# Kernel optimization log

Hardware: AMD Instinct MI355X
Metric: run time of the kernel (lower is better)

Reference implementation:

```python
import jax, jax.numpy as jnp
import numpy as np

EMB_DIM = 1024
N_HEAD = 16
HEAD_DIM = EMB_DIM // N_HEAD


def setup_inputs() -> dict:
    key = jax.random.key(0)
    k1, k2, k3, k4, k5 = jax.random.split(key, 5)
    x = jax.random.normal(k1, (4, 2048, EMB_DIM), dtype=jnp.float32)
    s = 1.0 / np.sqrt(EMB_DIM)
    W_qkv = jax.random.uniform(k2, (3 * EMB_DIM, EMB_DIM), minval=-s, maxval=s, dtype=jnp.float32)
    b_qkv = jax.random.uniform(k3, (3 * EMB_DIM,), minval=-s, maxval=s, dtype=jnp.float32)
    W_proj = jax.random.uniform(k4, (EMB_DIM, EMB_DIM), minval=-s, maxval=s, dtype=jnp.float32)
    b_proj = jax.random.uniform(k5, (EMB_DIM,), minval=-s, maxval=s, dtype=jnp.float32)
    return {"x": x, "W_qkv": W_qkv, "b_qkv": b_qkv, "W_proj": W_proj, "b_proj": b_proj}


def reference(x, W_qkv, b_qkv, W_proj, b_proj):
    B, S, E = x.shape
    H, D = N_HEAD, HEAD_DIM
    qkv = x @ W_qkv.T + b_qkv  # [B,S,3E]
    q, k, v = jnp.split(qkv, 3, axis=-1)
    # [B,S,E] -> [B,H,S,D]
    q = q.reshape(B, S, H, D).transpose(0, 2, 1, 3)
    k = k.reshape(B, S, H, D).transpose(0, 2, 1, 3)
    v = v.reshape(B, S, H, D).transpose(0, 2, 1, 3)
    scale = 1.0 / jnp.sqrt(jnp.asarray(D, dtype=x.dtype))
    scores = jnp.einsum('bhqd,bhkd->bhqk', q, k) * scale
    causal = jnp.tril(jnp.ones((S, S), dtype=bool))
    scores = jnp.where(causal, scores, jnp.asarray(-jnp.inf, dtype=scores.dtype))
    attn = jax.nn.softmax(scores, axis=-1)
    y = jnp.einsum('bhqk,bhkd->bhqd', attn, v)  # [B,H,S,D]
    y = y.transpose(0, 2, 1, 3).reshape(B, S, E)
    return y @ W_proj.T + b_proj
```

## Files before the change

kernel.cpp:

```cpp
#include <hip/hip_runtime.h>
#include <hip/hip_bf16.h>

typedef __attribute__((ext_vector_type(4))) float f32x4;
typedef __attribute__((ext_vector_type(16))) float f32x16;
typedef __attribute__((ext_vector_type(8))) __bf16 bf16x8;
typedef __attribute__((ext_vector_type(4))) unsigned int u32x4;

#define EMB 1024
#define NHEAD 16
#define HDIM 64
#define SEQ 2048
#define BATCH 4
#define NTOK 8192

__device__ __forceinline__ unsigned short f2bf(float f) {
    unsigned int u = __builtin_bit_cast(unsigned int, f);
    u = (u + 0x7fffu + ((u >> 16) & 1u)) >> 16;
    return (unsigned short)u;
}

__device__ __forceinline__ unsigned int cvt2_bf16(float lo, float hi) {
    unsigned short a = __builtin_bit_cast(unsigned short, (__bf16)lo);
    unsigned short b = __builtin_bit_cast(unsigned short, (__bf16)hi);
    return (unsigned int)a | ((unsigned int)b << 16);
}

__device__ __forceinline__ void permlane32_swap(unsigned int &x, unsigned int &y) {
    asm volatile("v_permlane32_swap_b32 %0, %1" : "+v"(x), "+v"(y));
}

__device__ __forceinline__ void async_copy16(const ushort* g, ushort* l) {
    __builtin_amdgcn_global_load_lds(
        (const __attribute__((address_space(1))) void*)g,
        (__attribute__((address_space(3))) void*)l,
        16, 0, 0);
}

__global__ void cvt_f32_bf16(const float4* __restrict__ in, ushort* __restrict__ out, int n4) {
    int i = blockIdx.x * 256 + threadIdx.x;
    if (i < n4) {
        float4 v = in[i];
        ushort4 o;
        o.x = f2bf(v.x); o.y = f2bf(v.y); o.z = f2bf(v.z); o.w = f2bf(v.w);
        ((ushort4*)out)[i] = o;
    }
}

#define GEMM_STAGE64(Asrc, Bsrc, m0, n0, kt)                                      \
    {                                                                             \
        _Pragma("unroll")                                                         \
        for (int j = 0; j < 2; ++j) {                                             \
            int row = wave * 32 + j * 16 + (lane >> 2);                           \
            int kc  = (lane & 3) ^ ((row >> 1) & 3);                              \
            const ushort* asrc = Asrc + (size_t)(m0 + row) * EMB + kt + kc * 8;   \
            const ushort* bsrc = Bsrc + (size_t)(n0 + row) * EMB + kt + kc * 8;   \
            async_copy16(asrc,      As0 + (wave * 32 + j * 16) * 32);             \
            async_copy16(asrc + 32, As1 + (wave * 32 + j * 16) * 32);             \
            async_copy16(bsrc,      Bs0 + (wave * 32 + j * 16) * 32);             \
            async_copy16(bsrc + 32, Bs1 + (wave * 32 + j * 16) * 32);             \
        }                                                                         \
    }

#define GEMM_BODY64(Asrc, Bsrc, m0, n0)                                           \
    f32x4 acc[4][4] = {};                                                         \
    for (int kt = 0; kt < EMB; kt += 64) {                                        \
        GEMM_STAGE64(Asrc, Bsrc, m0, n0, kt)                                      \
        __syncthreads();                                                          \
        _Pragma("unroll")                                                         \
        for (int hf = 0; hf < 2; ++hf) {                                          \
            const ushort* Ah = hf ? As1 : As0;                                    \
            const ushort* Bh = hf ? Bs1 : Bs0;                                    \
            bf16x8 a[4], b[4];                                                    \
            _Pragma("unroll")                                                     \
            for (int i = 0; i < 4; ++i) {                                         \
                int r = wm + i * 16 + col;                                        \
                a[i] = *(const bf16x8*)&Ah[r * 32 + (quad ^ ((r >> 1) & 3)) * 8]; \
                int c = wn + i * 16 + col;                                        \
                b[i] = *(const bf16x8*)&Bh[c * 32 + (quad ^ ((c >> 1) & 3)) * 8]; \
            }                                                                     \
            _Pragma("unroll")                                                     \
            for (int i = 0; i < 4; ++i)                                           \
                _Pragma("unroll")                                                 \
                for (int j = 0; j < 4; ++j)                                       \
                    acc[i][j] = __builtin_amdgcn_mfma_f32_16x16x32_bf16(          \
                        a[i], b[j], acc[i][j], 0, 0, 0);                          \
        }                                                                         \
        __syncthreads();                                                          \
    }

__global__ __launch_bounds__(256) void gemm_qk(
    const ushort* __restrict__ A,
    const ushort* __restrict__ W,
    const float*  __restrict__ bias,
    ushort* __restrict__ Qb, ushort* __restrict__ Kb)
{
    __shared__ ushort As0[128 * 32];
    __shared__ ushort As1[128 * 32];
    __shared__ ushort Bs0[128 * 32];
    __shared__ ushort Bs1[128 * 32];
    const int tid  = threadIdx.x;
    const int lane = tid & 63;
    const int wave = tid >> 6;
    const int col  = lane & 15;
    const int quad = lane >> 4;
    const int m0 = blockIdx.x * 128;
    const int n0 = blockIdx.y * 128;
    const int wm = (wave >> 1) * 64;
    const int wn = (wave & 1) * 64;

    GEMM_BODY64(A, W, m0, n0)

    #pragma unroll
    for (int i = 0; i < 4; ++i)
        #pragma unroll
        for (int j = 0; j < 4; ++j)
            #pragma unroll
            for (int r = 0; r < 4; ++r) {
                int m = m0 + wm + i * 16 + quad * 4 + r;
                int n = n0 + wn + j * 16 + col;
                float v = acc[i][j][r] + bias[n];
                unsigned short bv = f2bf(v);
                int e = n & 1023;
                int h = e >> 6, d = e & 63;
                int b = m >> 11, s = m & 2047;
                size_t bh = (size_t)(b * NHEAD + h);
                if (n < 1024) Qb[(bh * SEQ + s) * HDIM + d] = bv;
                else          Kb[(bh * SEQ + s) * HDIM + d] = bv;
            }
}

__global__ __launch_bounds__(256) void gemm_vt(
    const ushort* __restrict__ Wv,
    const ushort* __restrict__ X,
    const float*  __restrict__ bias,
    ushort* __restrict__ Vtx)
{
    __shared__ ushort As0[128 * 32];
    __shared__ ushort As1[128 * 32];
    __shared__ ushort Bs0[128 * 32];
    __shared__ ushort Bs1[128 * 32];
    const int tid  = threadIdx.x;
    const int lane = tid & 63;
    const int wave = tid >> 6;
    const int col  = lane & 15;
    const int quad = lane >> 4;
    const int m0 = blockIdx.x * 128;
    const int n0 = blockIdx.y * 128;
    const int wm = (wave >> 1) * 64;
    const int wn = (wave & 1) * 64;

    GEMM_BODY64(Wv, X, m0, n0)

    #pragma unroll
    for (int i = 0; i < 4; ++i)
        #pragma unroll
        for (int j = 0; j < 4; ++j)
            #pragma unroll
            for (int r = 0; r < 4; ++r) {
                int m = m0 + wm + i * 16 + quad * 4 + r;
                int n = n0 + wn + j * 16 + col;
                Vtx[(size_t)m * NTOK + n] = f2bf(acc[i][j][r] + bias[m]);
            }
}

__global__ __launch_bounds__(256) void gemm_proj(
    const ushort* __restrict__ A,
    const ushort* __restrict__ W,
    const float*  __restrict__ bias,
    float* __restrict__ out)
{
    __shared__ ushort As0[128 * 32];
    __shared__ ushort As1[128 * 32];
    __shared__ ushort Bs0[128 * 32];
    __shared__ ushort Bs1[128 * 32];
    const int tid  = threadIdx.x;
    const int lane = tid & 63;
    const int wave = tid >> 6;
    const int col  = lane & 15;
    const int quad = lane >> 4;
    const int m0 = blockIdx.x * 128;
    const int n0 = blockIdx.y * 128;
    const int wm = (wave >> 1) * 64;
    const int wn = (wave & 1) * 64;

    GEMM_BODY64(A, W, m0, n0)

    #pragma unroll
    for (int i = 0; i < 4; ++i)
        #pragma unroll
        for (int j = 0; j < 4; ++j)
            #pragma unroll
            for (int r = 0; r < 4; ++r) {
                int m = m0 + wm + i * 16 + quad * 4 + r;
                int n = n0 + wn + j * 16 + col;
                out[(size_t)m * EMB + n] = acc[i][j][r] + bias[n];
            }
}

__device__ __forceinline__ void attn_qtile(
    int qt, int b, int h, int lane, int wave,
    const ushort* __restrict__ Qh, const ushort* __restrict__ Kh,
    const ushort* __restrict__ Vh, ushort* __restrict__ Yb,
    ushort* __restrict__ Ks0, ushort* __restrict__ Ks1, ushort* __restrict__ Vs)
{
    const int ql = lane & 31;
    const int hi = lane >> 5;
    const int q0 = qt * 128 + wave * 32;
    const int qrow = q0 + ql;
    const float SC = 0.125f * 1.44269504f;

    bf16x8 qb[4];
    #pragma unroll
    for (int c = 0; c < 4; ++c)
        qb[c] = *(const bf16x8*)(Qh + (size_t)qrow * HDIM + c * 16 + hi * 8);

    f32x16 o2[2] = {};
    float lrun = 0.f;

    const int nk = qt + 1;
    for (int kt = 0; kt < nk; ++kt) {
        const int k0 = kt * 128;
        const bool last = (kt == nk - 1);

        {
            int srow = wave * 16 + (lane >> 2);
            #pragma unroll
            for (int rr = 0; rr < 2; ++rr) {
                int r = rr * 64 + srow;
                int kc = (lane & 3) ^ ((r >> 1) & 3);
                const ushort* src = Kh + (size_t)(k0 + r) * HDIM + kc * 8;
                async_copy16(src,      Ks0 + (rr * 64 + wave * 16) * 32);
                async_copy16(src + 32, Ks1 + (rr * 64 + wave * 16) * 32);
            }
            int kc = (lane & 3) ^ ((srow >> 1) & 3);
            const ushort* vsrc = Vh + (size_t)srow * NTOK + k0 + kc * 8;
            #pragma unroll
            for (int kq = 0; kq < 4; ++kq)
                async_copy16(vsrc + kq * 32, Vs + kq * 2048 + (wave * 16) * 32);
        }
        __syncthreads();

        f32x16 st[4];
        #pragma unroll
        for (int t = 0; t < 4; ++t) {
            f32x16 acc = {};
            #pragma unroll
            for (int c = 0; c < 4; ++c) {
                int row = t * 32 + ql;
                int swz = ((c & 1) * 2 + hi) ^ ((row >> 1) & 3);
                const ushort* Kbase = (c < 2) ? Ks0 : Ks1;
                bf16x8 kf = *(const bf16x8*)&Kbase[row * 32 + swz * 8];
                acc = __builtin_amdgcn_mfma_f32_32x32x16_bf16(kf, qb[c], acc, 0, 0, 0);
            }
            st[t] = acc;
        }

        if (last) {
            #pragma unroll
            for (int t = 0; t < 4; ++t)
                #pragma unroll
                for (int r = 0; r < 16; ++r) {
                    float pv = __builtin_amdgcn_exp2f(st[t][r] * SC);
                    int key = k0 + t * 32 + (r & 3) + 8 * (r >> 2) + 4 * hi;
                    pv = (key <= qrow) ? pv : 0.f;
                    st[t][r] = pv;
                    lrun += pv;
                }
        } else {
            #pragma unroll
            for (int t = 0; t < 4; ++t)
                #pragma unroll
                for (int r = 0; r < 16; ++r) {
                    float pv = __builtin_amdgcn_exp2f(st[t][r] * SC);
                    st[t][r] = pv;
                    lrun += pv;
                }
        }

        #pragma unroll
        for (int t = 0; t < 4; ++t) {
            unsigned int Ap[4], Bp[4];
            #pragma unroll
            for (int m = 0; m < 4; ++m) {
                Ap[m] = cvt2_bf16(st[t][4 * m],     st[t][4 * m + 1]);
                Bp[m] = cvt2_bf16(st[t][4 * m + 2], st[t][4 * m + 3]);
            }
            #pragma unroll
            for (int kc = 0; kc < 2; ++kc) {
                unsigned int xa = Ap[2 * kc], ya = Ap[2 * kc + 1];
                unsigned int xb = Bp[2 * kc], yb = Bp[2 * kc + 1];
                permlane32_swap(xa, ya);
                permlane32_swap(xb, yb);
                u32x4 pw; pw[0] = xa; pw[1] = xb; pw[2] = ya; pw[3] = yb;
                bf16x8 pf = __builtin_bit_cast(bf16x8, pw);
                #pragma unroll
                for (int dt = 0; dt < 2; ++dt) {
                    int row = dt * 32 + ql;
                    int swz = (kc * 2 + hi) ^ ((row >> 1) & 3);
                    bf16x8 vf = *(const bf16x8*)&Vs[t * 2048 + row * 32 + swz * 8];
                    o2[dt] = __builtin_amdgcn_mfma_f32_32x32x16_bf16(vf, pf, o2[dt], 0, 0, 0);
                }
            }
        }
        __syncthreads();
    }

    lrun += __shfl_xor(lrun, 32, 64);
    float inv = 1.f / lrun;
    size_t rbase = ((size_t)(b * SEQ + qrow)) * EMB + h * HDIM;
    #pragma unroll
    for (int dt = 0; dt < 2; ++dt)
        #pragma unroll
        for (int m = 0; m < 4; ++m) {
            int d = dt * 32 + 8 * m + 4 * hi;
            ushort4 s4;
            s4.x = f2bf(o2[dt][4 * m]     * inv);
            s4.y = f2bf(o2[dt][4 * m + 1] * inv);
            s4.z = f2bf(o2[dt][4 * m + 2] * inv);
            s4.w = f2bf(o2[dt][4 * m + 3] * inv);
            *(ushort4*)(Yb + rbase + d) = s4;
        }
}

__global__ __launch_bounds__(256, 2) void attn(
    const ushort* __restrict__ Qb, const ushort* __restrict__ Kb,
    const ushort* __restrict__ Vtx, ushort* __restrict__ Yb)
{
    __shared__ ushort Ks0[128 * 32];
    __shared__ ushort Ks1[128 * 32];
    __shared__ ushort Vs[4 * 64 * 32];
    const int lane = threadIdx.x & 63;
    const int wave = threadIdx.x >> 6;
    const int bh   = blockIdx.x & 63;
    const int pr   = blockIdx.x >> 6;

    const int b = bh >> 4, h = bh & 15;
    const ushort* Qh = Qb + (size_t)bh * SEQ * HDIM;
    const ushort* Kh = Kb + (size_t)bh * SEQ * HDIM;
    const ushort* Vh = Vtx + (size_t)(h * HDIM) * NTOK + b * SEQ;

    attn_qtile(15 - pr, b, h, lane, wave, Qh, Kh, Vh, Yb, Ks0, Ks1, Vs);
    __syncthreads();
    attn_qtile(pr,      b, h, lane, wave, Qh, Kh, Vh, Yb, Ks0, Ks1, Vs);
}

extern "C" void kernel_launch(void* const* d_in, const int* in_sizes, int n_in,
                              void* d_out, int out_size, void* d_ws, size_t ws_size,
                              hipStream_t stream) {
    const float* x      = (const float*)d_in[0];
    const float* W_qkv  = (const float*)d_in[1];
    const float* b_qkv  = (const float*)d_in[2];
    const float* W_proj = (const float*)d_in[3];
    const float* b_proj = (const float*)d_in[4];
    float* out = (float*)d_out;

    ushort* ws     = (ushort*)d_ws;
    ushort* Xb     = ws;
    ushort* Yb     = ws;
    ushort* Wqkvb  = ws + 8388608;
    ushort* Wprojb = ws + 11534336;
    ushort* Qb     = ws + 12582912;
    ushort* Kb     = ws + 20971520;
    ushort* Vtx    = ws + 29360128;

    cvt_f32_bf16<<<8192, 256, 0, stream>>>((const float4*)x,      Xb,     2097152);
    cvt_f32_bf16<<<3072, 256, 0, stream>>>((const float4*)W_qkv,  Wqkvb,  786432);
    cvt_f32_bf16<<<1024, 256, 0, stream>>>((const float4*)W_proj, Wprojb, 262144);

    gemm_qk<<<dim3(64, 16), 256, 0, stream>>>(Xb, Wqkvb, b_qkv, Qb, Kb);
    gemm_vt<<<dim3(8, 64), 256, 0, stream>>>(Wqkvb + (size_t)2048 * EMB, Xb,
                                             b_qkv + 2048, Vtx);
    attn<<<512, 256, 0, stream>>>(Qb, Kb, Vtx, Yb);
    gemm_proj<<<dim3(64, 8), 256, 0, stream>>>(Yb, Wprojb, b_proj, out);
}
```

Baseline: 244.7 us.

## Enlarge QK GEMM tiles to 256x256 with 512 threads and fuse conversion kernels

```diff
diff --git a/kernel.cpp b/kernel.cpp
--- a/kernel.cpp
+++ b/kernel.cpp
@@ -36,14 +36,23 @@
         16, 0, 0);
 }
 
-__global__ void cvt_f32_bf16(const float4* __restrict__ in, ushort* __restrict__ out, int n4) {
+#define XN4 2097152
+#define WQN4 786432
+#define WPN4 262144
+__global__ void cvt_all(const float4* __restrict__ x, const float4* __restrict__ wqkv,
+                        const float4* __restrict__ wproj,
+                        ushort* __restrict__ xb, ushort* __restrict__ wqkvb,
+                        ushort* __restrict__ wprojb) {
     int i = blockIdx.x * 256 + threadIdx.x;
-    if (i < n4) {
-        float4 v = in[i];
-        ushort4 o;
-        o.x = f2bf(v.x); o.y = f2bf(v.y); o.z = f2bf(v.z); o.w = f2bf(v.w);
-        ((ushort4*)out)[i] = o;
-    }
+    const float4* src; ushort* dst; int k;
+    if (i < XN4)                { src = x;     dst = xb;     k = i; }
+    else if (i < XN4 + WQN4)    { src = wqkv;  dst = wqkvb;  k = i - XN4; }
+    else if (i < XN4 + WQN4 + WPN4) { src = wproj; dst = wprojb; k = i - XN4 - WQN4; }
+    else return;
+    float4 v = src[k];
+    ushort4 o;
+    o.x = f2bf(v.x); o.y = f2bf(v.y); o.z = f2bf(v.z); o.w = f2bf(v.w);
+    ((ushort4*)dst)[k] = o;
 }
 
 #define GEMM_STAGE64(Asrc, Bsrc, m0, n0, kt)                                      \
@@ -88,30 +97,80 @@
         __syncthreads();                                                          \
     }
 
-__global__ __launch_bounds__(256) void gemm_qk(
+__global__ __launch_bounds__(512, 2) void gemm_qk(
     const ushort* __restrict__ A,
     const ushort* __restrict__ W,
     const float*  __restrict__ bias,
     ushort* __restrict__ Qb, ushort* __restrict__ Kb)
 {
-    __shared__ ushort As0[128 * 32];
-    __shared__ ushort As1[128 * 32];
-    __shared__ ushort Bs0[128 * 32];
-    __shared__ ushort Bs1[128 * 32];
+    extern __shared__ ushort lds[];
     const int tid  = threadIdx.x;
     const int lane = tid & 63;
     const int wave = tid >> 6;
     const int col  = lane & 15;
     const int quad = lane >> 4;
-    const int m0 = blockIdx.x * 128;
-    const int n0 = blockIdx.y * 128;
-    const int wm = (wave >> 1) * 64;
-    const int wn = (wave & 1) * 64;
-
-    GEMM_BODY64(A, W, m0, n0)
+    const int n0 = blockIdx.x * 256;
+    const int m0 = blockIdx.y * 256;
+    const int wm = (wave >> 2) * 128;
+    const int wn = (wave & 3) * 64;
+
+    f32x4 acc[8][4] = {};
+
+#define QK_STAGE(b_, kt)                                                          \
+    {                                                                             \
+        _Pragma("unroll")                                                         \
+        for (int j = 0; j < 2; ++j) {                                             \
+            int row = wave * 32 + j * 16 + (lane >> 2);                           \
+            int kc  = (lane & 3) ^ ((row >> 1) & 3);                              \
+            const ushort* asrc = A + (size_t)(m0 + row) * EMB + kt + kc * 8;      \
+            const ushort* bsrc = W + (size_t)(n0 + row) * EMB + kt + kc * 8;      \
+            ushort* db = (b_) + (wave * 32 + j * 16) * 32;                        \
+            async_copy16(asrc,      db);                                          \
+            async_copy16(asrc + 32, db + 8192);                                   \
+            async_copy16(bsrc,      db + 16384);                                  \
+            async_copy16(bsrc + 32, db + 24576);                                  \
+        }                                                                         \
+    }
+
+    QK_STAGE(lds, 0)
+    __syncthreads();
+
+    for (int ki = 0; ki < 16; ++ki) {
+        const int cur = ki & 1;
+        if (ki < 15) QK_STAGE(lds + (cur ^ 1) * 32768, (ki + 1) * 64)
+
+        const ushort* buf = lds + cur * 32768;
+        const ushort* A0 = buf;
+        const ushort* A1 = buf + 8192;
+        const ushort* B0 = buf + 16384;
+        const ushort* B1 = buf + 24576;
+
+        bf16x8 b0[4], b1[4];
+        #pragma unroll
+        for (int j = 0; j < 4; ++j) {
+            int c = wn + j * 16 + col;
+            int swz = (quad ^ ((c >> 1) & 3)) * 8;
+            b0[j] = *(const bf16x8*)&B0[c * 32 + swz];
+            b1[j] = *(const bf16x8*)&B1[c * 32 + swz];
+        }
+        #pragma unroll
+        for (int i = 0; i < 8; ++i) {
+            int r = wm + i * 16 + col;
+            int swz = (quad ^ ((r >> 1) & 3)) * 8;
+            bf16x8 a0 = *(const bf16x8*)&A0[r * 32 + swz];
+            bf16x8 a1 = *(const bf16x8*)&A1[r * 32 + swz];
+            #pragma unroll
+            for (int j = 0; j < 4; ++j) {
+                acc[i][j] = __builtin_amdgcn_mfma_f32_16x16x32_bf16(a0, b0[j], acc[i][j], 0, 0, 0);
+                acc[i][j] = __builtin_amdgcn_mfma_f32_16x16x32_bf16(a1, b1[j], acc[i][j], 0, 0, 0);
+            }
+        }
+        __syncthreads();
+    }
+#undef QK_STAGE
 
     #pragma unroll
-    for (int i = 0; i < 4; ++i)
+    for (int i = 0; i < 8; ++i)
         #pragma unroll
         for (int j = 0; j < 4; ++j)
             #pragma unroll
@@ -363,11 +422,13 @@
     ushort* Kb     = ws + 20971520;
     ushort* Vtx    = ws + 29360128;
 
-    cvt_f32_bf16<<<8192, 256, 0, stream>>>((const float4*)x,      Xb,     2097152);
-    cvt_f32_bf16<<<3072, 256, 0, stream>>>((const float4*)W_qkv,  Wqkvb,  786432);
-    cvt_f32_bf16<<<1024, 256, 0, stream>>>((const float4*)W_proj, Wprojb, 262144);
-
-    gemm_qk<<<dim3(64, 16), 256, 0, stream>>>(Xb, Wqkvb, b_qkv, Qb, Kb);
+    hipFuncSetAttribute((const void*)gemm_qk,
+                        hipFuncAttributeMaxDynamicSharedMemorySize, 131072);
+
+    cvt_all<<<12288, 256, 0, stream>>>((const float4*)x, (const float4*)W_qkv,
+                                       (const float4*)W_proj, Xb, Wqkvb, Wprojb);
+
+    gemm_qk<<<dim3(8, 32), 512, 131072, stream>>>(Xb, Wqkvb, b_qkv, Qb, Kb);
     gemm_vt<<<dim3(8, 64), 256, 0, stream>>>(Wqkvb + (size_t)2048 * EMB, Xb,
                                              b_qkv + 2048, Vtx);
     attn<<<512, 256, 0, stream>>>(Qb, Kb, Vtx, Yb);
```

Measured after the change: 239.8 us. 1.02x faster.
